# Optimization experiments

Hardware: AMD Instinct MI355X
Metric: run time of the kernel (lower is better)

The kernel has to match this reference:

```python
import jax, jax.numpy as jnp
import numpy as np

HIDDEN = 512
BATCH = 64
SEQ = 1024
FUTURE = 16


def setup_inputs() -> dict:
    key = jax.random.key(0)
    ks = jax.random.split(key, 12)
    s = 0.05  # small init to keep the un-squashed LSTM recurrence stable
    H = HIDDEN
    inp = {
        "x": jax.random.normal(ks[0], (BATCH, SEQ), dtype=jnp.float32),
        # cell 1: input_length=1
        "W1": jax.random.normal(ks[1], (4 * H, 1), dtype=jnp.float32) * s,
        "bW1": jax.random.normal(ks[2], (4 * H,), dtype=jnp.float32) * s,
        "U1": jax.random.normal(ks[3], (4 * H, H), dtype=jnp.float32) * s,
        "bU1": jax.random.normal(ks[4], (4 * H,), dtype=jnp.float32) * s,
        # cell 2: input_length=H
        "W2": jax.random.normal(ks[5], (4 * H, H), dtype=jnp.float32) * s,
        "bW2": jax.random.normal(ks[6], (4 * H,), dtype=jnp.float32) * s,
        "U2": jax.random.normal(ks[7], (4 * H, H), dtype=jnp.float32) * s,
        "bU2": jax.random.normal(ks[8], (4 * H,), dtype=jnp.float32) * s,
        # output head: Linear(H, 1)
        "lw": jax.random.normal(ks[9], (1, H), dtype=jnp.float32) * s,
        "lb": jax.random.normal(ks[10], (1,), dtype=jnp.float32) * s,
        "future": FUTURE,
    }
    return inp


def _cell(x_t, h, c, W, bW, U, bU):
    # NOTE: faithful to source — NO sigmoid/tanh on the gates, only tanh on c_t.
    gates = x_t @ W.T + bW + h @ U.T + bU            # [B, 4H]
    i_t, f_t, g_t, o_t = jnp.split(gates, 4, axis=-1)
    c_t = f_t * c + i_t * g_t
    h_t = o_t * jnp.tanh(c_t)
    return h_t, c_t


def reference(x, W1, bW1, U1, bU1, W2, bW2, U2, bU2, lw, lb, future):
    B = x.shape[0]
    H = U1.shape[1]
    zeros = jnp.zeros((B, H), dtype=x.dtype)
    init = (zeros, zeros, zeros, zeros, jnp.zeros((B, 1), dtype=x.dtype))

    def run(carry, x_t):
        h1, c1, h2, c2, _ = carry
        h1, c1 = _cell(x_t, h1, c1, W1, bW1, U1, bU1)
        h2, c2 = _cell(h1, h2, c2, W2, bW2, U2, bU2)
        out = h2 @ lw.T + lb                          # [B, 1]
        return (h1, c1, h2, c2, out), out

    # teacher-forced pass over the observed sequence
    xs = x.T[:, :, None]                              # [T, B, 1]
    carry, outs = jax.lax.scan(run, init, xs)         # outs: [T, B, 1]

    if future > 0:
        def run_future(carry, _):
            return run(carry, carry[4])
        carry, outs_f = jax.lax.scan(run_future, carry, None, length=future)
        outs = jnp.concatenate([outs, outs_f], axis=0)

    return outs[:, :, 0].T                            # [B, T+future]
```

## Files before the change

kernel.cpp:

```cpp
#include <hip/hip_runtime.h>
#include <math.h>

#define HID 512
#define B 64
#define SEQT 1024
#define FUT 16
#define TT (SEQT + FUT)
#define NWG 256
#define TPB 512
#define TPB1 1024
#define NWAVE1 16
#define JPW 2
#define HB (HID * B)
#define BLOBF 12288

typedef __attribute__((ext_vector_type(2))) float f2;

#define WS_H1_F   512
#define WS_H2_F   (WS_H1_F + 2 * HB)
#define WS_BLOB_F (WS_H2_F + 2 * HB)
#define WS_XT_F   (WS_BLOB_F + NWG * BLOBF)
#define WS_TOT_F  (WS_XT_F + SEQT * B)
#define WS_PART_F WS_TOT_F
#define WS_TOT2_F (WS_PART_F + (size_t)SEQT * NWG * B)

__device__ inline void pub_store(float* p, float v) {
  (void)__hip_atomic_exchange(p, v, __ATOMIC_RELAXED, __HIP_MEMORY_SCOPE_AGENT);
}

__device__ inline void gbar5(int* bb, int wg, int bar) {
  __builtin_amdgcn_s_waitcnt(0);
  __syncthreads();
  const int tid = threadIdx.x;
  if (tid == 0) {
    __hip_atomic_store(bb + wg, bar, __ATOMIC_RELAXED, __HIP_MEMORY_SCOPE_AGENT);
    __builtin_amdgcn_fence(__ATOMIC_ACQUIRE, "agent");
  }
  if (tid < 64) {
    for (;;) {
      int a = __hip_atomic_load(bb + tid,       __ATOMIC_RELAXED, __HIP_MEMORY_SCOPE_AGENT);
      int b = __hip_atomic_load(bb + 64  + tid, __ATOMIC_RELAXED, __HIP_MEMORY_SCOPE_AGENT);
      int c = __hip_atomic_load(bb + 128 + tid, __ATOMIC_RELAXED, __HIP_MEMORY_SCOPE_AGENT);
      int d = __hip_atomic_load(bb + 192 + tid, __ATOMIC_RELAXED, __HIP_MEMORY_SCOPE_AGENT);
      if (__all(a >= bar && b >= bar && c >= bar && d >= bar)) break;
      __builtin_amdgcn_s_sleep(1);
    }
  }
  __syncthreads();
}

__global__ void __launch_bounds__(256) prep_ws(
    const float* __restrict__ x,
    const float* __restrict__ U1, const float* __restrict__ W2,
    const float* __restrict__ U2, float* __restrict__ ws)
{
  const int idx = blockIdx.x * blockDim.x + threadIdx.x;
  if (idx < WS_BLOB_F) ws[idx] = 0.0f;
  {
    const int i2 = idx - WS_BLOB_F;
    if (i2 >= 0 && i2 < NWG * BLOBF) {
      const int wg  = i2 / BLOBF;
      const int off = i2 - wg * BLOBF;
      const int j0  = wg * JPW;
      float v;
      if (off < 4096) {
        const int k = off >> 3, r = off & 7;
        const int row = (r >> 1) * HID + j0 + (r & 1);
        v = U1[(size_t)row * HID + k];
      } else {
        const int o2 = off - 4096;
        const int k = o2 >> 4, rr = o2 & 15;
        const int r = rr & 7;
        const int row = (r >> 1) * HID + j0 + (r & 1);
        v = (rr < 8) ? W2[(size_t)row * HID + k] : U2[(size_t)row * HID + k];
      }
      ws[WS_BLOB_F + i2] = v;
    }
  }
  {
    const int i3 = idx - WS_XT_F;
    if (i3 >= 0 && i3 < SEQT * B) {
      const int t = i3 >> 6, b = i3 & 63;
      ws[WS_XT_F + i3] = x[(size_t)b * SEQT + t];
    }
  }
}

__global__ void __launch_bounds__(TPB1, 1) rnn_main(
    const float* __restrict__ W1, const float* __restrict__ bW1,
    const float* __restrict__ bU1,
    const float* __restrict__ bW2, const float* __restrict__ bU2,
    const float* __restrict__ lw, const float* __restrict__ lb,
    float* __restrict__ out,
    int* __restrict__ bb,
    float* __restrict__ h1b, float* __restrict__ h2b,
    const float* __restrict__ wbl, const float* __restrict__ xT,
    float* __restrict__ part, int defer)
{
  __shared__ float wlds[BLOBF];
  __shared__ float red[NWAVE1][8][B];
  __shared__ float outred[NWAVE1][B];
  __shared__ float c1s[JPW][B], c2s[JPW][B];
  __shared__ float pout[JPW][B];
  __shared__ float w1c[8], bs1[8], bs2[8], lwc[JPW];

  const int wg   = blockIdx.x;
  const int j0   = wg * JPW;
  const int tid  = threadIdx.x;
  const int lane = tid & 63;
  const int wvu  = __builtin_amdgcn_readfirstlane(tid >> 6);

  {
    const float4* gsrc = (const float4*)(wbl + (size_t)wg * BLOBF);
    float4* ldst = (float4*)wlds;
    #pragma unroll
    for (int i = 0; i < BLOBF / 4 / TPB1; ++i)
      ldst[i * TPB1 + tid] = gsrc[i * TPB1 + tid];
  }
  if (tid < JPW * B) { c1s[tid >> 6][lane] = 0.f; c2s[tid >> 6][lane] = 0.f; }
  if (tid < 8) {
    const int g = tid >> 1, jl = tid & 1;
    const int row = g * HID + j0 + jl;
    w1c[tid] = W1[row];
    bs1[tid] = bW1[row] + bU1[row];
    bs2[tid] = bW2[row] + bU2[row];
  }
  if (tid < JPW) lwc[tid] = lw[j0 + tid];
  __syncthreads();

  const float* wl1 = wlds + wvu * 256;
  const float* wl2 = wlds + 4096 + wvu * 512;
  const float lbv = lb[0];

  float4 H1[8], Q[8];
  #pragma unroll
  for (int i = 0; i < 8; ++i) H1[i] = make_float4(0.f, 0.f, 0.f, 0.f);

  int bar = 0;
  for (int t = 0; t < TT; ++t) {
    float*       h1new = h1b + (t & 1) * HB;
    const float* h2old = h2b + ((t + 1) & 1) * HB;
    float*       h2new = h2b + (t & 1) * HB;

    float xvpref = 0.f;
    if (tid < JPW * B && t < SEQT) xvpref = xT[(size_t)t * B + lane];

    {
      f2 a01 = {0.f, 0.f}, a23 = {0.f, 0.f}, a45 = {0.f, 0.f}, a67 = {0.f, 0.f};
      #pragma unroll
      for (int c = 0; c < 8; ++c) {
        const float hh[4] = {H1[c].x, H1[c].y, H1[c].z, H1[c].w};
        #pragma unroll
        for (int j = 0; j < 4; ++j) {
          const float4 wA = *(const float4*)(wl1 + c * 32 + j * 8);
          const float4 wB = *(const float4*)(wl1 + c * 32 + j * 8 + 4);
          const f2 hs = {hh[j], hh[j]};
          const f2 wA0 = {wA.x, wA.y}, wA1 = {wA.z, wA.w};
          const f2 wB0 = {wB.x, wB.y}, wB1 = {wB.z, wB.w};
          a01 = __builtin_elementwise_fma(wA0, hs, a01);
          a23 = __builtin_elementwise_fma(wA1, hs, a23);
          a45 = __builtin_elementwise_fma(wB0, hs, a45);
          a67 = __builtin_elementwise_fma(wB1, hs, a67);
        }
      }
      red[wvu][0][lane] = a01.x; red[wvu][1][lane] = a01.y;
      red[wvu][2][lane] = a23.x; red[wvu][3][lane] = a23.y;
      red[wvu][4][lane] = a45.x; red[wvu][5][lane] = a45.y;
      red[wvu][6][lane] = a67.x; red[wvu][7][lane] = a67.y;
    }
    __syncthreads();

    if (tid < JPW * B) {
      const int jl = tid >> 6, b = tid & 63;
      const float xv = (t < SEQT) ? xvpref : out[(size_t)b * TT + (t - 1)];
      float gate[4];
      #pragma unroll
      for (int g = 0; g < 4; ++g) {
        const int r = g * 2 + jl;
        float s = bs1[r] + xv * w1c[r];
        #pragma unroll
        for (int w = 0; w < NWAVE1; ++w) s += red[w][r][b];
        gate[g] = s;
      }
      const float c = gate[1] * c1s[jl][b] + gate[0] * gate[2];
      c1s[jl][b] = c;
      const int j = j0 + jl;
      pub_store(&h1new[(size_t)(j >> 2) * (B * 4) + b * 4 + (j & 3)],
                gate[3] * tanhf(c));
    }

    ++bar;
    gbar5(bb, wg, bar);

    if (!defer && wg == (t & 127) && t >= 1 && t <= SEQT - 1) {
      const float4* hb2 = (const float4*)h2old + (size_t)(wvu * 8) * B + lane;
      const float4* lw4 = (const float4*)lw + wvu * 8;
      float p = 0.f;
      #pragma unroll
      for (int i = 0; i < 8; ++i) {
        const float4 hv = hb2[i * B];
        const float4 wv = lw4[i];
        p = fmaf(wv.x, hv.x, p); p = fmaf(wv.y, hv.y, p);
        p = fmaf(wv.z, hv.z, p); p = fmaf(wv.w, hv.w, p);
      }
      outred[wvu][lane] = p;
      __syncthreads();
      if (tid < B) {
        float o = lbv;
        #pragma unroll
        for (int s = 0; s < NWAVE1; ++s) o += outred[s][tid];
        pub_store(&out[(size_t)tid * TT + (t - 1)], o);
      }
      __syncthreads();
    }

    {
      const float4* pp4 = (const float4*)h1new + (size_t)(wvu * 8) * B + lane;
      const float4* qq4 = (const float4*)h2old + (size_t)(wvu * 8) * B + lane;
      #pragma unroll
      for (int i = 0; i < 8; ++i) H1[i] = pp4[i * B];
      #pragma unroll
      for (int i = 0; i < 8; ++i) Q[i] = qq4[i * B];
      f2 a01 = {0.f, 0.f}, a23 = {0.f, 0.f}, a45 = {0.f, 0.f}, a67 = {0.f, 0.f};
      #pragma unroll
      for (int c = 0; c < 8; ++c) {
        const float hp_[4] = {H1[c].x, H1[c].y, H1[c].z, H1[c].w};
        const float hq_[4] = {Q[c].x, Q[c].y, Q[c].z, Q[c].w};
        #pragma unroll
        for (int j = 0; j < 4; ++j) {
          const float4 w0 = *(const float4*)(wl2 + c * 64 + j * 16);
          const float4 w1 = *(const float4*)(wl2 + c * 64 + j * 16 + 4);
          const float4 w2 = *(const float4*)(wl2 + c * 64 + j * 16 + 8);
          const float4 w3 = *(const float4*)(wl2 + c * 64 + j * 16 + 12);
          const f2 hs1 = {hp_[j], hp_[j]};
          const f2 hs2 = {hq_[j], hq_[j]};
          const f2 w0a = {w0.x, w0.y}, w0b = {w0.z, w0.w};
          const f2 w1a = {w1.x, w1.y}, w1b = {w1.z, w1.w};
          const f2 w2a = {w2.x, w2.y}, w2b = {w2.z, w2.w};
          const f2 w3a = {w3.x, w3.y}, w3b = {w3.z, w3.w};
          a01 = __builtin_elementwise_fma(w0a, hs1, a01);
          a23 = __builtin_elementwise_fma(w0b, hs1, a23);
          a45 = __builtin_elementwise_fma(w1a, hs1, a45);
          a67 = __builtin_elementwise_fma(w1b, hs1, a67);
          a01 = __builtin_elementwise_fma(w2a, hs2, a01);
          a23 = __builtin_elementwise_fma(w2b, hs2, a23);
          a45 = __builtin_elementwise_fma(w3a, hs2, a45);
          a67 = __builtin_elementwise_fma(w3b, hs2, a67);
        }
      }
      red[wvu][0][lane] = a01.x; red[wvu][1][lane] = a01.y;
      red[wvu][2][lane] = a23.x; red[wvu][3][lane] = a23.y;
      red[wvu][4][lane] = a45.x; red[wvu][5][lane] = a45.y;
      red[wvu][6][lane] = a67.x; red[wvu][7][lane] = a67.y;
    }
    __syncthreads();

    if (tid < JPW * B) {
      const int jl = tid >> 6, b = tid & 63;
      float gate[4];
      #pragma unroll
      for (int g = 0; g < 4; ++g) {
        const int r = g * 2 + jl;
        float s = bs2[r];
        #pragma unroll
        for (int w = 0; w < NWAVE1; ++w) s += red[w][r][b];
        gate[g] = s;
      }
      const float c = gate[1] * c2s[jl][b] + gate[0] * gate[2];
      c2s[jl][b] = c;
      const float h2v = gate[3] * tanhf(c);
      const int j = j0 + jl;
      pub_store(&h2new[(size_t)(j >> 2) * (B * 4) + b * 4 + (j & 3)], h2v);
      if (defer && t < SEQT) pout[jl][b] = lwc[jl] * h2v;
    }
    __syncthreads();

    if (defer && t < SEQT && tid < B) {
      pub_store(&part[((size_t)t * NWG + wg) * B + tid],
                pout[0][tid] + pout[1][tid]);
    }

    if (t >= SEQT - 1) {
      ++bar;
      gbar5(bb, wg, bar);
      if (wg == 0) {
        const float4* hb2 = (const float4*)h2new + (size_t)(wvu * 8) * B + lane;
        const float4* lw4 = (const float4*)lw + wvu * 8;
        float p = 0.f;
        #pragma unroll
        for (int i = 0; i < 8; ++i) {
          const float4 hv = hb2[i * B];
          const float4 wv = lw4[i];
          p = fmaf(wv.x, hv.x, p); p = fmaf(wv.y, hv.y, p);
          p = fmaf(wv.z, hv.z, p); p = fmaf(wv.w, hv.w, p);
        }
        outred[wvu][lane] = p;
        __syncthreads();
        if (tid < B) {
          float o = lbv;
          #pragma unroll
          for (int s = 0; s < NWAVE1; ++s) o += outred[s][tid];
          pub_store(&out[(size_t)tid * TT + t], o);
        }
        __syncthreads();
      }
      ++bar;
      gbar5(bb, wg, bar);
    }
  }

  if (defer) {
    ++bar;
    gbar5(bb, wg, bar);
    for (int tt = wg; tt < SEQT - 1; tt += NWG) {
      const float* pp = part + ((size_t)tt * NWG + wvu * 16) * B + lane;
      float s = 0.f;
      #pragma unroll
      for (int i = 0; i < 16; ++i) s += pp[i * B];
      outred[wvu][lane] = s;
      __syncthreads();
      if (tid < B) {
        float o = lbv;
        #pragma unroll
        for (int v = 0; v < NWAVE1; ++v) o += outred[v][tid];
        out[(size_t)tid * TT + tt] = o;
      }
      __syncthreads();
    }
  }
}

__device__ inline void gbar(int* cnt, int target) {
  __syncthreads();
  if (threadIdx.x == 0) {
    __threadfence();
    __hip_atomic_fetch_add(cnt, 1, __ATOMIC_RELEASE, __HIP_MEMORY_SCOPE_AGENT);
    while (__hip_atomic_load(cnt, __ATOMIC_ACQUIRE, __HIP_MEMORY_SCOPE_AGENT) < target) {
      __builtin_amdgcn_s_sleep(2);
    }
  }
  __syncthreads();
}

__global__ void __launch_bounds__(TPB) zero_ws(float* ws, int n) {
  int i = blockIdx.x * blockDim.x + threadIdx.x;
  if (i < n) ws[i] = 0.0f;
}

__global__ void __launch_bounds__(TPB) rnn_fallback(
    const float* __restrict__ x,
    const float* __restrict__ W1, const float* __restrict__ bW1,
    const float* __restrict__ U1, const float* __restrict__ bU1,
    const float* __restrict__ W2, const float* __restrict__ bW2,
    const float* __restrict__ U2, const float* __restrict__ bU2,
    const float* __restrict__ lw, const float* __restrict__ lb,
    float* out, float* ws)
{
  __shared__ float red[8][8][B];
  __shared__ float outred[8][B];
  __shared__ float c1s[JPW][B], c2s[JPW][B];
  __shared__ float w1c[8], bs1[8], bs2[8];

  int* cnt   = (int*)ws;
  float* h1b = ws + 16;
  float* h2b = h1b + 2 * HB;

  const int wg   = blockIdx.x;
  const int j0   = wg * JPW;
  const int tid  = threadIdx.x;
  const int lane = tid & 63;
  const int wvu  = __builtin_amdgcn_readfirstlane(tid >> 6);
  const int kb   = wvu << 6;

  if (tid < JPW * B) { c1s[tid >> 6][lane] = 0.f; c2s[tid >> 6][lane] = 0.f; }
  if (tid < 8) {
    const int g = tid >> 1, jl = tid & 1;
    const int row = g * HID + j0 + jl;
    w1c[tid] = W1[row];
    bs1[tid] = bW1[row] + bU1[row];
    bs2[tid] = bW2[row] + bU2[row];
  }
  __syncthreads();

  const float* u1p[8]; const float* w2p[8]; const float* u2p[8];
  #pragma unroll
  for (int r = 0; r < 8; ++r) {
    const int row = (r >> 1) * HID + j0 + (r & 1);
    u1p[r] = U1 + (size_t)row * HID + kb;
    w2p[r] = W2 + (size_t)row * HID + kb;
    u2p[r] = U2 + (size_t)row * HID + kb;
  }
  const float lbv = lb[0];

  int bar = 0;
  for (int t = 0; t < TT; ++t) {
    const float* h1old = h1b + ((t + 1) & 1) * HB;
    float*       h1new = h1b + (t & 1) * HB;
    const float* h2old = h2b + ((t + 1) & 1) * HB;
    float*       h2new = h2b + (t & 1) * HB;

    {
      const float* hp = h1old + (size_t)kb * B;
      float a0=0.f,a1=0.f,a2=0.f,a3=0.f,a4=0.f,a5=0.f,a6=0.f,a7=0.f;
      #pragma unroll 8
      for (int k = 0; k < 64; ++k) {
        const float hv = hp[k * B + lane];
        a0 = fmaf(u1p[0][k], hv, a0); a1 = fmaf(u1p[1][k], hv, a1);
        a2 = fmaf(u1p[2][k], hv, a2); a3 = fmaf(u1p[3][k], hv, a3);
        a4 = fmaf(u1p[4][k], hv, a4); a5 = fmaf(u1p[5][k], hv, a5);
        a6 = fmaf(u1p[6][k], hv, a6); a7 = fmaf(u1p[7][k], hv, a7);
      }
      red[wvu][0][lane]=a0; red[wvu][1][lane]=a1; red[wvu][2][lane]=a2; red[wvu][3][lane]=a3;
      red[wvu][4][lane]=a4; red[wvu][5][lane]=a5; red[wvu][6][lane]=a6; red[wvu][7][lane]=a7;
    }
    __syncthreads();

    if (tid < JPW * B) {
      const int jl = tid >> 6, b = tid & 63;
      const float xv = (t < SEQT) ? x[(size_t)b * SEQT + t]
                                  : out[(size_t)b * TT + (t - 1)];
      float gate[4];
      #pragma unroll
      for (int g = 0; g < 4; ++g) {
        const int r = g * 2 + jl;
        float s = bs1[r] + xv * w1c[r];
        #pragma unroll
        for (int w = 0; w < 8; ++w) s += red[w][r][b];
        gate[g] = s;
      }
      const float c = gate[1] * c1s[jl][b] + gate[0] * gate[2];
      c1s[jl][b] = c;
      h1new[(size_t)(j0 + jl) * B + b] = gate[3] * tanhf(c);
    }

    ++bar;
    gbar(cnt, NWG * bar);

    if (wg == 0 && t >= 1 && t <= SEQT - 1) {
      const float* hb2 = h2old + (size_t)(wvu * 64) * B;
      const float* lwp = lw + wvu * 64;
      float p = 0.f;
      #pragma unroll 8
      for (int j = 0; j < 64; ++j) p = fmaf(lwp[j], hb2[j * B + lane], p);
      outred[wvu][lane] = p;
      __syncthreads();
      if (tid < B) {
        float o = lbv;
        #pragma unroll
        for (int s = 0; s < 8; ++s) o += outred[s][tid];
        out[(size_t)tid * TT + (t - 1)] = o;
      }
      __syncthreads();
    }

    {
      const float* h1p = h1new + (size_t)kb * B;
      const float* h2p = h2old + (size_t)kb * B;
      float s0=0.f,s1=0.f,s2=0.f,s3=0.f,s4=0.f,s5=0.f,s6=0.f,s7=0.f;
      float q0=0.f,q1=0.f,q2=0.f,q3=0.f,q4=0.f,q5=0.f,q6=0.f,q7=0.f;
      #pragma unroll 4
      for (int k = 0; k < 64; ++k) {
        const float h1v = h1p[k * B + lane];
        const float h2v = h2p[k * B + lane];
        s0 = fmaf(w2p[0][k], h1v, s0); q0 = fmaf(u2p[0][k], h2v, q0);
        s1 = fmaf(w2p[1][k], h1v, s1); q1 = fmaf(u2p[1][k], h2v, q1);
        s2 = fmaf(w2p[2][k], h1v, s2); q2 = fmaf(u2p[2][k], h2v, q2);
        s3 = fmaf(w2p[3][k], h1v, s3); q3 = fmaf(u2p[3][k], h2v, q3);
        s4 = fmaf(w2p[4][k], h1v, s4); q4 = fmaf(u2p[4][k], h2v, q4);
        s5 = fmaf(w2p[5][k], h1v, s5); q5 = fmaf(u2p[5][k], h2v, q5);
        s6 = fmaf(w2p[6][k], h1v, s6); q6 = fmaf(u2p[6][k], h2v, q6);
        s7 = fmaf(w2p[7][k], h1v, s7); q7 = fmaf(u2p[7][k], h2v, q7);
      }
      red[wvu][0][lane]=s0+q0; red[wvu][1][lane]=s1+q1;
      red[wvu][2][lane]=s2+q2; red[wvu][3][lane]=s3+q3;
      red[wvu][4][lane]=s4+q4; red[wvu][5][lane]=s5+q5;
      red[wvu][6][lane]=s6+q6; red[wvu][7][lane]=s7+q7;
    }
    __syncthreads();

    if (tid < JPW * B) {
      const int jl = tid >> 6, b = tid & 63;
      float gate[4];
      #pragma unroll
      for (int g = 0; g < 4; ++g) {
        const int r = g * 2 + jl;
        float s = bs2[r];
        #pragma unroll
        for (int w = 0; w < 8; ++w) s += red[w][r][b];
        gate[g] = s;
      }
      const float c = gate[1] * c2s[jl][b] + gate[0] * gate[2];
      c2s[jl][b] = c;
      h2new[(size_t)(j0 + jl) * B + b] = gate[3] * tanhf(c);
    }
    __syncthreads();

    if (t >= SEQT - 1) {
      ++bar;
      gbar(cnt, NWG * bar);
      if (wg == 0) {
        const float* hb2 = h2new + (size_t)(wvu * 64) * B;
        const float* lwp = lw + wvu * 64;
        float p = 0.f;
        #pragma unroll 8
        for (int j = 0; j < 64; ++j) p = fmaf(lwp[j], hb2[j * B + lane], p);
        outred[wvu][lane] = p;
        __syncthreads();
        if (tid < B) {
          float o = lbv;
          #pragma unroll
          for (int s = 0; s < 8; ++s) o += outred[s][tid];
          out[(size_t)tid * TT + t] = o;
        }
        __syncthreads();
      }
      ++bar;
      gbar(cnt, NWG * bar);
    }
  }
}

extern "C" void kernel_launch(void* const* d_in, const int* in_sizes, int n_in,
                              void* d_out, int out_size, void* d_ws, size_t ws_size,
                              hipStream_t stream) {
  (void)in_sizes; (void)n_in; (void)out_size;
  const float* x   = (const float*)d_in[0];
  const float* W1  = (const float*)d_in[1];
  const float* bW1 = (const float*)d_in[2];
  const float* U1  = (const float*)d_in[3];
  const float* bU1 = (const float*)d_in[4];
  const float* W2  = (const float*)d_in[5];
  const float* bW2 = (const float*)d_in[6];
  const float* U2  = (const float*)d_in[7];
  const float* bU2 = (const float*)d_in[8];
  const float* lw  = (const float*)d_in[9];
  const float* lb  = (const float*)d_in[10];

  float* out = (float*)d_out;
  float* ws  = (float*)d_ws;

  if (ws_size >= (size_t)WS_TOT_F * sizeof(float)) {
    const int defer = (ws_size >= WS_TOT2_F * sizeof(float)) ? 1 : 0;
    prep_ws<<<(WS_TOT_F + 255) / 256, 256, 0, stream>>>(x, U1, W2, U2, ws);
    rnn_main<<<NWG, TPB1, 0, stream>>>(W1, bW1, bU1, bW2, bU2, lw, lb, out,
                                       (int*)ws, ws + WS_H1_F, ws + WS_H2_F,
                                       ws + WS_BLOB_F, ws + WS_XT_F,
                                       ws + WS_PART_F, defer);
  } else {
    const int nzero = 16 + 4 * HID * B;
    zero_ws<<<(nzero + TPB - 1) / TPB, TPB, 0, stream>>>(ws, nzero);
    rnn_fallback<<<NWG, TPB, 0, stream>>>(x, W1, bW1, U1, bU1,
                                          W2, bW2, U2, bU2, lw, lb, out, ws);
  }
}
```

Before: 11.64 ms.

## Re-tile hidden-state layout to 2x2 (k,batch) blocks and split K across half-waves

Changes the global h1/h2 exchange layout from [k/4][b][4] to 2k-by-2b float4 tiles, so each lane owns two batch columns and half the wave's K range. The gate matvec then broadcasts a weight scalar against a batch pair, with 8 accumulators instead of 4, and the reduction buffer gains a K-half dimension that the gate stage sums. The aim is to halve the per-lane LDS weight reads relative to FMAs and to make the packed FMAs more regular. In exchange the reduction doubles its LDS reads, and the output-head dot products need lane-parity selects.

```diff
diff --git a/kernel.cpp b/kernel.cpp
--- a/kernel.cpp
+++ b/kernel.cpp
@@ -15,6 +15,8 @@
 #define BLOBF 12288
 
 typedef __attribute__((ext_vector_type(2))) float f2;
+
+__device__ inline f2 dupf(float v) { return (f2){v, v}; }
 
 #define WS_H1_F   512
 #define WS_H2_F   (WS_H1_F + 2 * HB)
@@ -98,7 +100,7 @@
     float* __restrict__ part, int defer)
 {
   __shared__ float wlds[BLOBF];
-  __shared__ float red[NWAVE1][8][B];
+  __shared__ float red[NWAVE1][2][8][B];
   __shared__ float outred[NWAVE1][B];
   __shared__ float c1s[JPW][B], c2s[JPW][B];
   __shared__ float pout[JPW][B];
@@ -109,6 +111,8 @@
   const int tid  = threadIdx.x;
   const int lane = tid & 63;
   const int wvu  = __builtin_amdgcn_readfirstlane(tid >> 6);
+  const int bp   = lane & 31;
+  const int kh   = lane >> 5;
 
   {
     const float4* gsrc = (const float4*)(wbl + (size_t)wg * BLOBF);
@@ -117,7 +121,7 @@
     for (int i = 0; i < BLOBF / 4 / TPB1; ++i)
       ldst[i * TPB1 + tid] = gsrc[i * TPB1 + tid];
   }
-  if (tid < JPW * B) { c1s[tid >> 6][lane] = 0.f; c2s[tid >> 6][lane] = 0.f; }
+  if (tid < JPW * B) { c1s[tid >> 6][tid & 63] = 0.f; c2s[tid >> 6][tid & 63] = 0.f; }
   if (tid < 8) {
     const int g = tid >> 1, jl = tid & 1;
     const int row = g * HID + j0 + jl;
@@ -132,6 +136,8 @@
   const float* wl2 = wlds + 4096 + wvu * 512;
   const float lbv = lb[0];
 
+  const int kq0 = wvu * 16 + kh * 8;
+
   float4 H1[8], Q[8];
   #pragma unroll
   for (int i = 0; i < 8; ++i) H1[i] = make_float4(0.f, 0.f, 0.f, 0.f);
@@ -143,30 +149,46 @@
     float*       h2new = h2b + (t & 1) * HB;
 
     float xvpref = 0.f;
-    if (tid < JPW * B && t < SEQT) xvpref = xT[(size_t)t * B + lane];
+    if (tid < JPW * B && t < SEQT) xvpref = xT[(size_t)t * B + (tid & 63)];
 
     {
-      f2 a01 = {0.f, 0.f}, a23 = {0.f, 0.f}, a45 = {0.f, 0.f}, a67 = {0.f, 0.f};
-      #pragma unroll
-      for (int c = 0; c < 8; ++c) {
-        const float hh[4] = {H1[c].x, H1[c].y, H1[c].z, H1[c].w};
-        #pragma unroll
-        for (int j = 0; j < 4; ++j) {
-          const float4 wA = *(const float4*)(wl1 + c * 32 + j * 8);
-          const float4 wB = *(const float4*)(wl1 + c * 32 + j * 8 + 4);
-          const f2 hs = {hh[j], hh[j]};
-          const f2 wA0 = {wA.x, wA.y}, wA1 = {wA.z, wA.w};
-          const f2 wB0 = {wB.x, wB.y}, wB1 = {wB.z, wB.w};
-          a01 = __builtin_elementwise_fma(wA0, hs, a01);
-          a23 = __builtin_elementwise_fma(wA1, hs, a23);
-          a45 = __builtin_elementwise_fma(wB0, hs, a45);
-          a67 = __builtin_elementwise_fma(wB1, hs, a67);
+      f2 ac0 = {0.f, 0.f}, ac1 = {0.f, 0.f}, ac2 = {0.f, 0.f}, ac3 = {0.f, 0.f};
+      f2 ac4 = {0.f, 0.f}, ac5 = {0.f, 0.f}, ac6 = {0.f, 0.f}, ac7 = {0.f, 0.f};
+      #pragma unroll
+      for (int i = 0; i < 8; ++i) {
+        const f2 he = {H1[i].x, H1[i].y};
+        const f2 ho = {H1[i].z, H1[i].w};
+        const float* wp = wl1 + (kh * 16 + 2 * i) * 8;
+        {
+          const float4 wA = *(const float4*)(wp);
+          const float4 wB = *(const float4*)(wp + 4);
+          ac0 = __builtin_elementwise_fma(dupf(wA.x), he, ac0);
+          ac1 = __builtin_elementwise_fma(dupf(wA.y), he, ac1);
+          ac2 = __builtin_elementwise_fma(dupf(wA.z), he, ac2);
+          ac3 = __builtin_elementwise_fma(dupf(wA.w), he, ac3);
+          ac4 = __builtin_elementwise_fma(dupf(wB.x), he, ac4);
+          ac5 = __builtin_elementwise_fma(dupf(wB.y), he, ac5);
+          ac6 = __builtin_elementwise_fma(dupf(wB.z), he, ac6);
+          ac7 = __builtin_elementwise_fma(dupf(wB.w), he, ac7);
         }
-      }
-      red[wvu][0][lane] = a01.x; red[wvu][1][lane] = a01.y;
-      red[wvu][2][lane] = a23.x; red[wvu][3][lane] = a23.y;
-      red[wvu][4][lane] = a45.x; red[wvu][5][lane] = a45.y;
-      red[wvu][6][lane] = a67.x; red[wvu][7][lane] = a67.y;
+        {
+          const float4 wC = *(const float4*)(wp + 8);
+          const float4 wD = *(const float4*)(wp + 12);
+          ac0 = __builtin_elementwise_fma(dupf(wC.x), ho, ac0);
+          ac1 = __builtin_elementwise_fma(dupf(wC.y), ho, ac1);
+          ac2 = __builtin_elementwise_fma(dupf(wC.z), ho, ac2);
+          ac3 = __builtin_elementwise_fma(dupf(wC.w), ho, ac3);
+          ac4 = __builtin_elementwise_fma(dupf(wD.x), ho, ac4);
+          ac5 = __builtin_elementwise_fma(dupf(wD.y), ho, ac5);
+          ac6 = __builtin_elementwise_fma(dupf(wD.z), ho, ac6);
+          ac7 = __builtin_elementwise_fma(dupf(wD.w), ho, ac7);
+        }
+      }
+      f2* rb = (f2*)(&red[wvu][kh][0][0]);
+      rb[0 * 32 + bp] = ac0; rb[1 * 32 + bp] = ac1;
+      rb[2 * 32 + bp] = ac2; rb[3 * 32 + bp] = ac3;
+      rb[4 * 32 + bp] = ac4; rb[5 * 32 + bp] = ac5;
+      rb[6 * 32 + bp] = ac6; rb[7 * 32 + bp] = ac7;
     }
     __syncthreads();
 
@@ -179,13 +201,13 @@
         const int r = g * 2 + jl;
         float s = bs1[r] + xv * w1c[r];
         #pragma unroll
-        for (int w = 0; w < NWAVE1; ++w) s += red[w][r][b];
+        for (int w = 0; w < NWAVE1; ++w) s += red[w][0][r][b] + red[w][1][r][b];
         gate[g] = s;
       }
       const float c = gate[1] * c1s[jl][b] + gate[0] * gate[2];
       c1s[jl][b] = c;
       const int j = j0 + jl;
-      pub_store(&h1new[(size_t)(j >> 2) * (B * 4) + b * 4 + (j & 3)],
+      pub_store(&h1new[(size_t)((j >> 1) * 32 + (b >> 1)) * 4 + (j & 1) * 2 + (b & 1)],
                 gate[3] * tanhf(c));
     }
 
@@ -193,15 +215,17 @@
     gbar5(bb, wg, bar);
 
     if (!defer && wg == (t & 127) && t >= 1 && t <= SEQT - 1) {
-      const float4* hb2 = (const float4*)h2old + (size_t)(wvu * 8) * B + lane;
-      const float4* lw4 = (const float4*)lw + wvu * 8;
+      const int b = lane;
+      const float4* hb2 = (const float4*)h2old + (size_t)(wvu * 16) * 32 + (b >> 1);
+      const float* lwp = lw + wvu * 32;
       float p = 0.f;
       #pragma unroll
-      for (int i = 0; i < 8; ++i) {
-        const float4 hv = hb2[i * B];
-        const float4 wv = lw4[i];
-        p = fmaf(wv.x, hv.x, p); p = fmaf(wv.y, hv.y, p);
-        p = fmaf(wv.z, hv.z, p); p = fmaf(wv.w, hv.w, p);
+      for (int ii = 0; ii < 16; ++ii) {
+        const float4 v = hb2[ii * 32];
+        const float hk0 = (b & 1) ? v.y : v.x;
+        const float hk1 = (b & 1) ? v.w : v.z;
+        p = fmaf(lwp[2 * ii], hk0, p);
+        p = fmaf(lwp[2 * ii + 1], hk1, p);
       }
       outred[wvu][lane] = p;
       __syncthreads();
@@ -215,43 +239,71 @@
     }
 
     {
-      const float4* pp4 = (const float4*)h1new + (size_t)(wvu * 8) * B + lane;
-      const float4* qq4 = (const float4*)h2old + (size_t)(wvu * 8) * B + lane;
-      #pragma unroll
-      for (int i = 0; i < 8; ++i) H1[i] = pp4[i * B];
-      #pragma unroll
-      for (int i = 0; i < 8; ++i) Q[i] = qq4[i * B];
-      f2 a01 = {0.f, 0.f}, a23 = {0.f, 0.f}, a45 = {0.f, 0.f}, a67 = {0.f, 0.f};
-      #pragma unroll
-      for (int c = 0; c < 8; ++c) {
-        const float hp_[4] = {H1[c].x, H1[c].y, H1[c].z, H1[c].w};
-        const float hq_[4] = {Q[c].x, Q[c].y, Q[c].z, Q[c].w};
-        #pragma unroll
-        for (int j = 0; j < 4; ++j) {
-          const float4 w0 = *(const float4*)(wl2 + c * 64 + j * 16);
-          const float4 w1 = *(const float4*)(wl2 + c * 64 + j * 16 + 4);
-          const float4 w2 = *(const float4*)(wl2 + c * 64 + j * 16 + 8);
-          const float4 w3 = *(const float4*)(wl2 + c * 64 + j * 16 + 12);
-          const f2 hs1 = {hp_[j], hp_[j]};
-          const f2 hs2 = {hq_[j], hq_[j]};
-          const f2 w0a = {w0.x, w0.y}, w0b = {w0.z, w0.w};
-          const f2 w1a = {w1.x, w1.y}, w1b = {w1.z, w1.w};
-          const f2 w2a = {w2.x, w2.y}, w2b = {w2.z, w2.w};
-          const f2 w3a = {w3.x, w3.y}, w3b = {w3.z, w3.w};
-          a01 = __builtin_elementwise_fma(w0a, hs1, a01);
-          a23 = __builtin_elementwise_fma(w0b, hs1, a23);
-          a45 = __builtin_elementwise_fma(w1a, hs1, a45);
-          a67 = __builtin_elementwise_fma(w1b, hs1, a67);
-          a01 = __builtin_elementwise_fma(w2a, hs2, a01);
-          a23 = __builtin_elementwise_fma(w2b, hs2, a23);
-          a45 = __builtin_elementwise_fma(w3a, hs2, a45);
-          a67 = __builtin_elementwise_fma(w3b, hs2, a67);
+      const float4* pp4 = (const float4*)h1new + (size_t)kq0 * 32 + bp;
+      const float4* qq4 = (const float4*)h2old + (size_t)kq0 * 32 + bp;
+      #pragma unroll
+      for (int i = 0; i < 8; ++i) H1[i] = pp4[i * 32];
+      #pragma unroll
+      for (int i = 0; i < 8; ++i) Q[i] = qq4[i * 32];
+      f2 ac0 = {0.f, 0.f}, ac1 = {0.f, 0.f}, ac2 = {0.f, 0.f}, ac3 = {0.f, 0.f};
+      f2 ac4 = {0.f, 0.f}, ac5 = {0.f, 0.f}, ac6 = {0.f, 0.f}, ac7 = {0.f, 0.f};
+      #pragma unroll
+      for (int i = 0; i < 8; ++i) {
+        const f2 h1e = {H1[i].x, H1[i].y};
+        const f2 h1o = {H1[i].z, H1[i].w};
+        const f2 qe  = {Q[i].x,  Q[i].y};
+        const f2 qo  = {Q[i].z,  Q[i].w};
+        const float* wp = wl2 + (kh * 16 + 2 * i) * 16;
+        {
+          const float4 wA = *(const float4*)(wp);
+          const float4 wB = *(const float4*)(wp + 4);
+          ac0 = __builtin_elementwise_fma(dupf(wA.x), h1e, ac0);
+          ac1 = __builtin_elementwise_fma(dupf(wA.y), h1e, ac1);
+          ac2 = __builtin_elementwise_fma(dupf(wA.z), h1e, ac2);
+          ac3 = __builtin_elementwise_fma(dupf(wA.w), h1e, ac3);
+          ac4 = __builtin_elementwise_fma(dupf(wB.x), h1e, ac4);
+          ac5 = __builtin_elementwise_fma(dupf(wB.y), h1e, ac5);
+          ac6 = __builtin_elementwise_fma(dupf(wB.z), h1e, ac6);
+          ac7 = __builtin_elementwise_fma(dupf(wB.w), h1e, ac7);
+          const float4 uA = *(const float4*)(wp + 8);
+          const float4 uB = *(const float4*)(wp + 12);
+          ac0 = __builtin_elementwise_fma(dupf(uA.x), qe, ac0);
+          ac1 = __builtin_elementwise_fma(dupf(uA.y), qe, ac1);
+          ac2 = __builtin_elementwise_fma(dupf(uA.z), qe, ac2);
+          ac3 = __builtin_elementwise_fma(dupf(uA.w), qe, ac3);
+          ac4 = __builtin_elementwise_fma(dupf(uB.x), qe, ac4);
+          ac5 = __builtin_elementwise_fma(dupf(uB.y), qe, ac5);
+          ac6 = __builtin_elementwise_fma(dupf(uB.z), qe, ac6);
+          ac7 = __builtin_elementwise_fma(dupf(uB.w), qe, ac7);
         }
-      }
-      red[wvu][0][lane] = a01.x; red[wvu][1][lane] = a01.y;
-      red[wvu][2][lane] = a23.x; red[wvu][3][lane] = a23.y;
-      red[wvu][4][lane] = a45.x; red[wvu][5][lane] = a45.y;
-      red[wvu][6][lane] = a67.x; red[wvu][7][lane] = a67.y;
+        {
+          const float4 wC = *(const float4*)(wp + 16);
+          const float4 wD = *(const float4*)(wp + 20);
+          ac0 = __builtin_elementwise_fma(dupf(wC.x), h1o, ac0);
+          ac1 = __builtin_elementwise_fma(dupf(wC.y), h1o, ac1);
+          ac2 = __builtin_elementwise_fma(dupf(wC.z), h1o, ac2);
+          ac3 = __builtin_elementwise_fma(dupf(wC.w), h1o, ac3);
+          ac4 = __builtin_elementwise_fma(dupf(wD.x), h1o, ac4);
+          ac5 = __builtin_elementwise_fma(dupf(wD.y), h1o, ac5);
+          ac6 = __builtin_elementwise_fma(dupf(wD.z), h1o, ac6);
+          ac7 = __builtin_elementwise_fma(dupf(wD.w), h1o, ac7);
+          const float4 uC = *(const float4*)(wp + 24);
+          const float4 uD = *(const float4*)(wp + 28);
+          ac0 = __builtin_elementwise_fma(dupf(uC.x), qo, ac0);
+          ac1 = __builtin_elementwise_fma(dupf(uC.y), qo, ac1);
+          ac2 = __builtin_elementwise_fma(dupf(uC.z), qo, ac2);
+          ac3 = __builtin_elementwise_fma(dupf(uC.w), qo, ac3);
+          ac4 = __builtin_elementwise_fma(dupf(uD.x), qo, ac4);
+          ac5 = __builtin_elementwise_fma(dupf(uD.y), qo, ac5);
+          ac6 = __builtin_elementwise_fma(dupf(uD.z), qo, ac6);
+          ac7 = __builtin_elementwise_fma(dupf(uD.w), qo, ac7);
+        }
+      }
+      f2* rb = (f2*)(&red[wvu][kh][0][0]);
+      rb[0 * 32 + bp] = ac0; rb[1 * 32 + bp] = ac1;
+      rb[2 * 32 + bp] = ac2; rb[3 * 32 + bp] = ac3;
+      rb[4 * 32 + bp] = ac4; rb[5 * 32 + bp] = ac5;
+      rb[6 * 32 + bp] = ac6; rb[7 * 32 + bp] = ac7;
     }
     __syncthreads();
 
@@ -263,14 +315,14 @@
         const int r = g * 2 + jl;
         float s = bs2[r];
         #pragma unroll
-        for (int w = 0; w < NWAVE1; ++w) s += red[w][r][b];
+        for (int w = 0; w < NWAVE1; ++w) s += red[w][0][r][b] + red[w][1][r][b];
         gate[g] = s;
       }
       const float c = gate[1] * c2s[jl][b] + gate[0] * gate[2];
       c2s[jl][b] = c;
       const float h2v = gate[3] * tanhf(c);
       const int j = j0 + jl;
-      pub_store(&h2new[(size_t)(j >> 2) * (B * 4) + b * 4 + (j & 3)], h2v);
+      pub_store(&h2new[(size_t)((j >> 1) * 32 + (b >> 1)) * 4 + (j & 1) * 2 + (b & 1)], h2v);
       if (defer && t < SEQT) pout[jl][b] = lwc[jl] * h2v;
     }
     __syncthreads();
@@ -284,15 +336,17 @@
       ++bar;
       gbar5(bb, wg, bar);
       if (wg == 0) {
-        const float4* hb2 = (const float4*)h2new + (size_t)(wvu * 8) * B + lane;
-        const float4* lw4 = (const float4*)lw + wvu * 8;
+        const int b = lane;
+        const float4* hb2 = (const float4*)h2new + (size_t)(wvu * 16) * 32 + (b >> 1);
+        const float* lwp = lw + wvu * 32;
         float p = 0.f;
         #pragma unroll
-        for (int i = 0; i < 8; ++i) {
-          const float4 hv = hb2[i * B];
-          const float4 wv = lw4[i];
-          p = fmaf(wv.x, hv.x, p); p = fmaf(wv.y, hv.y, p);
-          p = fmaf(wv.z, hv.z, p); p = fmaf(wv.w, hv.w, p);
+        for (int ii = 0; ii < 16; ++ii) {
+          const float4 v = hb2[ii * 32];
+          const float hk0 = (b & 1) ? v.y : v.x;
+          const float hk1 = (b & 1) ? v.w : v.z;
+          p = fmaf(lwp[2 * ii], hk0, p);
+          p = fmaf(lwp[2 * ii + 1], hk1, p);
         }
         outred[wvu][lane] = p;
         __syncthreads();
```

New measurement: 14.00 ms. +20.2%, slower.
